# Optimization experiments

Hardware: AMD Instinct MI355X
Metric: run time of the kernel (lower is better)

## Reference

```python
import jax, jax.numpy as jnp
import numpy as np

B, HQ, HKV, D = 32, 32, 8, 128
BLOCK_SIZE, MAX_BLOCKS = 16, 128
NUM_BLOCKS = B * MAX_BLOCKS
LMAX = MAX_BLOCKS * BLOCK_SIZE  # 2048 max context per sequence
ROPE_BASE = 10000.0


def _rope(x, pos):
    """Apply rotary embedding. x: [B, H, D], pos: [B] int positions."""
    half = D // 2
    inv_freq = 1.0 / (ROPE_BASE ** (jnp.arange(0, D, 2, dtype=jnp.float32) / D))  # [D/2]
    freqs = pos.astype(jnp.float32)[:, None] * inv_freq[None, :]  # [B, D/2]
    emb = jnp.concatenate([freqs, freqs], axis=-1)                # [B, D]
    cos = jnp.cos(emb)[:, None, :]  # [B, 1, D]
    sin = jnp.sin(emb)[:, None, :]
    x1, x2 = x[..., :half], x[..., half:]
    rotated = jnp.concatenate([-x2, x1], axis=-1)
    return x * cos + rotated * sin


def setup_inputs() -> dict:
    key = jax.random.key(0)
    ks = jax.random.split(key, 6)
    query = jax.random.normal(ks[0], (B, HQ, D), jnp.float32)
    new_k = jax.random.normal(ks[1], (B, HKV, D), jnp.float32)
    new_v = jax.random.normal(ks[2], (B, HKV, D), jnp.float32)
    k_cache = jax.random.normal(ks[3], (NUM_BLOCKS, BLOCK_SIZE, HKV, D), jnp.float32)
    v_cache = jax.random.normal(ks[4], (NUM_BLOCKS, BLOCK_SIZE, HKV, D), jnp.float32)
    # each sequence owns a disjoint contiguous range of blocks
    block_table = jnp.arange(B * MAX_BLOCKS, dtype=jnp.int32).reshape(B, MAX_BLOCKS)
    context_lens = jax.random.randint(ks[5], (B,), 1, LMAX - 1).astype(jnp.int32)
    return dict(query=query, new_k=new_k, new_v=new_v, k_cache=k_cache,
                v_cache=v_cache, block_table=block_table, context_lens=context_lens)


def reference(query, new_k, new_v, k_cache, v_cache, block_table, context_lens):
    scale = 1.0 / D ** 0.5
    pos = context_lens  # new token position for each sequence, [B]

    # RoPE on the decode-step query and key (seq_len == 1 per sequence)
    q = _rope(query, pos)      # [B, HQ, D]
    k_new = _rope(new_k, pos)  # [B, HKV, D]

    # flatten paged cache to [NUM_BLOCKS*BLOCK_SIZE, HKV, D]
    kc = k_cache.reshape(-1, HKV, D)
    vc = v_cache.reshape(-1, HKV, D)

    # paged KV-cache append: slot = block_table[b, pos//bs]*bs + pos%bs
    blk_new = jnp.take_along_axis(block_table, (pos // BLOCK_SIZE)[:, None], axis=1)[:, 0]
    slot = blk_new * BLOCK_SIZE + pos % BLOCK_SIZE  # [B]
    kc = kc.at[slot].set(k_new)
    vc = vc.at[slot].set(new_v)

    # gather per-sequence K/V via block table: [B, LMAX, HKV, D]
    p = jnp.arange(LMAX, dtype=jnp.int32)
    blks = block_table[:, p // BLOCK_SIZE]                 # [B, LMAX]
    idx = blks * BLOCK_SIZE + (p % BLOCK_SIZE)[None, :]    # [B, LMAX]
    keys = kc[idx]
    vals = vc[idx]

    # GQA attention over valid context (lengths = context_lens + 1 after append)
    lens = pos + 1
    g = HQ // HKV
    qg = q.reshape(B, HKV, g, D)
    scores = jnp.einsum('bkgd,blkd->bkgl', qg, keys) * scale  # [B, HKV, g, LMAX]
    mask = p[None, :] < lens[:, None]  # [B, LMAX]
    scores = jnp.where(mask[:, None, None, :], scores, -jnp.inf)
    w = jax.nn.softmax(scores, axis=-1)
    out = jnp.einsum('bkgl,blkd->bkgd', w, vals)
    return out.reshape(B, HQ, D)
```

## Files before the change

### kernel.cpp

```cpp
#include <hip/hip_runtime.h>
#include <math.h>

#define BATCH 32
#define HQ 32
#define HKV 8
#define DHEAD 128
#define BS 16
#define MAXB 128
#define G 4
#define CHUNK 256
#define MAXCH 8
#define NW 4
#define NT (NW * 64)

#define NSLOT (BATCH * HKV * MAXCH)

typedef float v2f __attribute__((ext_vector_type(2)));

__device__ __forceinline__ v2f pk_fma(v2f a, v2f b, v2f c) {
    v2f d;
    asm("v_pk_fma_f32 %0, %1, %2, %3" : "=v"(d) : "v"(a), "v"(b), "v"(c));
    return d;
}
__device__ __forceinline__ v2f pk_mul(v2f a, v2f b) {
    v2f d;
    asm("v_pk_mul_f32 %0, %1, %2" : "=v"(d) : "v"(a), "v"(b));
    return d;
}

#define ROR4(N, x0, x1, x2, x3)                                                   \
    asm("s_nop 1\n\t"                                                             \
        "v_add_f32_dpp %0, %0, %0 row_ror:" #N " row_mask:0xf bank_mask:0xf\n\t"  \
        "v_add_f32_dpp %1, %1, %1 row_ror:" #N " row_mask:0xf bank_mask:0xf\n\t"  \
        "v_add_f32_dpp %2, %2, %2 row_ror:" #N " row_mask:0xf bank_mask:0xf\n\t"  \
        "v_add_f32_dpp %3, %3, %3 row_ror:" #N " row_mask:0xf bank_mask:0xf"      \
        : "+v"(x0), "+v"(x1), "+v"(x2), "+v"(x3))

__global__ __launch_bounds__(NT) void paged_attn_chunk(
    const float* __restrict__ query,
    const float* __restrict__ new_k,
    const float* __restrict__ new_v,
    const float* __restrict__ k_cache,
    const float* __restrict__ v_cache,
    const int*   __restrict__ block_table,
    const int*   __restrict__ context_lens,
    float*       __restrict__ wsacc,
    float*       __restrict__ wsl)
{
    const int c   = blockIdx.x & (MAXCH - 1);
    const int bkv = blockIdx.x >> 3;
    const int kv  = bkv & 7;
    const int b   = bkv >> 3;

    const int pos = context_lens[b];
    const int len = pos + 1;
    const int c0  = c * CHUNK;
    if (c0 >= len) return;

    const int tid  = threadIdx.x;
    const int w    = tid >> 6;
    const int lane = tid & 63;
    const int grp  = lane >> 4;
    const int sub  = lane & 15;

    __shared__ float s_cos[64], s_sin[64];
    __shared__ float s_q[G][DHEAD];
    __shared__ float s_knew[DHEAD], s_vnew[DHEAD];
    __shared__ int   s_bt[CHUNK / BS];
    __shared__ float s_wacc[NW][G][DHEAD];
    __shared__ float s_wl[NW][G];

    if (tid < 64) {
        float invf = exp2f((float)tid * -0.20762050593046014f);
        float ang  = (float)pos * invf;
        s_cos[tid] = cosf(ang);
        s_sin[tid] = sinf(ang);
    }
    __syncthreads();

    const float scale = 0.08838834764831845f;

    for (int idx = tid; idx < G * DHEAD; idx += NT) {
        int h = idx >> 7, d = idx & 127;
        const float* qp = query + ((size_t)b * HQ + kv * G + h) * DHEAD;
        float x = qp[d], r;
        if (d < 64) r = x * s_cos[d]      - qp[d + 64] * s_sin[d];
        else        r = x * s_cos[d - 64] + qp[d - 64] * s_sin[d - 64];
        s_q[h][d] = r * scale;
    }
    if (tid < DHEAD) {
        int d = tid;
        const float* kp = new_k + ((size_t)b * HKV + kv) * DHEAD;
        float x = kp[d], r;
        if (d < 64) r = x * s_cos[d]      - kp[d + 64] * s_sin[d];
        else        r = x * s_cos[d - 64] + kp[d - 64] * s_sin[d - 64];
        s_knew[d] = r;
    } else if (tid < 2 * DHEAD) {
        int d = tid - DHEAD;
        s_vnew[d] = new_v[((size_t)b * HKV + kv) * DHEAD + d];
    }
    if (tid < CHUNK / BS) s_bt[tid] = block_table[b * MAXB + (c0 >> 4) + tid];
    __syncthreads();

    v2f q2[G][4];
    #pragma unroll
    for (int h = 0; h < G; h++)
        #pragma unroll
        for (int j = 0; j < 4; j++)
            q2[h][j] = v2f{s_q[h][sub * 8 + 2 * j], s_q[h][sub * 8 + 2 * j + 1]};

    v2f acc2[G][4];
    float l[G];
    #pragma unroll
    for (int h = 0; h < G; h++) {
        l[h] = 0.f;
        #pragma unroll
        for (int j = 0; j < 4; j++) acc2[h][j] = v2f{0.f, 0.f};
    }

    const size_t lofs = (size_t)kv * DHEAD + sub * 8;

    const int base = c0 + w * 64;
    int rem = len - base;
    int a = rem < 0 ? 0 : (rem > 64 ? 64 : rem);
    int nfull = a >> 2;
    int tail  = a & 3;

#define BODY(GUARDED)                                                          \
    {                                                                          \
        int slot = w * 64 + it * 4 + grp;                                      \
        int pi   = c0 + slot;                                                  \
        bool act = !(GUARDED) || (grp < tail);                                 \
        v2f k2[4], u2[4];                                                      \
        _Pragma("unroll")                                                      \
        for (int j = 0; j < 4; j++) { k2[j] = v2f{0.f, 0.f}; u2[j] = v2f{0.f, 0.f}; } \
        if (act) {                                                             \
            int blk = s_bt[slot >> 4];                                         \
            size_t row = (size_t)blk * (BS * HKV * DHEAD)                      \
                       + (size_t)(slot & 15) * (HKV * DHEAD) + lofs;           \
            float4 ka = *(const float4*)(k_cache + row);                       \
            float4 kb = *(const float4*)(k_cache + row + 4);                   \
            float4 va = *(const float4*)(v_cache + row);                       \
            float4 vb = *(const float4*)(v_cache + row + 4);                   \
            if (pi == pos) {                                                   \
                ka = *(const float4*)(s_knew + sub * 8);                       \
                kb = *(const float4*)(s_knew + sub * 8 + 4);                   \
                va = *(const float4*)(s_vnew + sub * 8);                       \
                vb = *(const float4*)(s_vnew + sub * 8 + 4);                   \
            }                                                                  \
            k2[0] = v2f{ka.x, ka.y}; k2[1] = v2f{ka.z, ka.w};                  \
            k2[2] = v2f{kb.x, kb.y}; k2[3] = v2f{kb.z, kb.w};                  \
            u2[0] = v2f{va.x, va.y}; u2[1] = v2f{va.z, va.w};                  \
            u2[2] = v2f{vb.x, vb.y}; u2[3] = v2f{vb.z, vb.w};                  \
        }                                                                      \
        float dt0, dt1, dt2, dt3;                                              \
        {                                                                      \
            v2f d0 = pk_fma(q2[0][3], k2[3], pk_fma(q2[0][2], k2[2],           \
                     pk_fma(q2[0][1], k2[1], pk_mul(q2[0][0], k2[0]))));       \
            v2f d1 = pk_fma(q2[1][3], k2[3], pk_fma(q2[1][2], k2[2],           \
                     pk_fma(q2[1][1], k2[1], pk_mul(q2[1][0], k2[0]))));       \
            v2f d2 = pk_fma(q2[2][3], k2[3], pk_fma(q2[2][2], k2[2],           \
                     pk_fma(q2[2][1], k2[1], pk_mul(q2[2][0], k2[0]))));       \
            v2f d3 = pk_fma(q2[3][3], k2[3], pk_fma(q2[3][2], k2[2],           \
                     pk_fma(q2[3][1], k2[1], pk_mul(q2[3][0], k2[0]))));       \
            dt0 = d0.x + d0.y; dt1 = d1.x + d1.y;                              \
            dt2 = d2.x + d2.y; dt3 = d3.x + d3.y;                              \
        }                                                                      \
        ROR4(8, dt0, dt1, dt2, dt3);                                           \
        ROR4(4, dt0, dt1, dt2, dt3);                                           \
        ROR4(2, dt0, dt1, dt2, dt3);                                           \
        ROR4(1, dt0, dt1, dt2, dt3);                                           \
        if (act) {                                                             \
            float wg0 = __expf(dt0), wg1 = __expf(dt1);                        \
            float wg2 = __expf(dt2), wg3 = __expf(dt3);                        \
            l[0] += wg0; l[1] += wg1; l[2] += wg2; l[3] += wg3;                \
            v2f w0 = v2f{wg0, wg0}, w1 = v2f{wg1, wg1};                        \
            v2f w2 = v2f{wg2, wg2}, w3 = v2f{wg3, wg3};                        \
            _Pragma("unroll")                                                  \
            for (int j = 0; j < 4; j++) {                                      \
                acc2[0][j] = pk_fma(w0, u2[j], acc2[0][j]);                    \
                acc2[1][j] = pk_fma(w1, u2[j], acc2[1][j]);                    \
                acc2[2][j] = pk_fma(w2, u2[j], acc2[2][j]);                    \
                acc2[3][j] = pk_fma(w3, u2[j], acc2[3][j]);                    \
            }                                                                  \
        }                                                                      \
    }

    #pragma unroll 2
    for (int it = 0; it < nfull; it++) BODY(false)
    if (tail) { int it = nfull; BODY(true) }
#undef BODY

    #pragma unroll
    for (int h = 0; h < G; h++) {
        l[h] += __shfl_xor(l[h], 16, 64);
        l[h] += __shfl_xor(l[h], 32, 64);
        #pragma unroll
        for (int j = 0; j < 4; j++) {
            float ax = acc2[h][j].x, ay = acc2[h][j].y;
            ax += __shfl_xor(ax, 16, 64); ax += __shfl_xor(ax, 32, 64);
            ay += __shfl_xor(ay, 16, 64); ay += __shfl_xor(ay, 32, 64);
            acc2[h][j] = v2f{ax, ay};
        }
    }
    if (lane < 16) {
        #pragma unroll
        for (int h = 0; h < G; h++)
            #pragma unroll
            for (int j = 0; j < 4; j++) {
                s_wacc[w][h][sub * 8 + 2 * j]     = acc2[h][j].x;
                s_wacc[w][h][sub * 8 + 2 * j + 1] = acc2[h][j].y;
            }
    }
    if (lane == 0) {
        #pragma unroll
        for (int h = 0; h < G; h++) s_wl[w][h] = l[h];
    }
    __syncthreads();

    const size_t slot_base = (size_t)blockIdx.x * (G * DHEAD);
    for (int idx = tid; idx < G * DHEAD; idx += NT) {
        float s = s_wacc[0][idx >> 7][idx & 127] + s_wacc[1][idx >> 7][idx & 127]
                + s_wacc[2][idx >> 7][idx & 127] + s_wacc[3][idx >> 7][idx & 127];
        wsacc[slot_base + idx] = s;
    }
    if (tid < G) {
        wsl[(size_t)blockIdx.x * G + tid] =
            s_wl[0][tid] + s_wl[1][tid] + s_wl[2][tid] + s_wl[3][tid];
    }
}

__global__ __launch_bounds__(512) void paged_attn_combine(
    const int*   __restrict__ context_lens,
    const float* __restrict__ wsacc,
    const float* __restrict__ wsl,
    float*       __restrict__ out)
{
    const int bkv = blockIdx.x;
    const int kv  = bkv & 7;
    const int b   = bkv >> 3;
    const int t   = threadIdx.x;
    const int h   = t >> 7;
    const int d   = t & 127;

    const int len = context_lens[b] + 1;
    const int nch = (len + CHUNK - 1) >> 8;

    float asum = 0.f, lsum = 0.f;
    for (int cc = 0; cc < nch; cc++) {
        asum += wsacc[((size_t)bkv * MAXCH + cc) * (G * DHEAD) + t];
        lsum += wsl[((size_t)bkv * MAXCH + cc) * G + h];
    }
    out[((size_t)b * HQ + kv * G + h) * DHEAD + d] = asum / lsum;
}

extern "C" void kernel_launch(void* const* d_in, const int* in_sizes, int n_in,
                              void* d_out, int out_size, void* d_ws, size_t ws_size,
                              hipStream_t stream) {
    const float* query        = (const float*)d_in[0];
    const float* new_k        = (const float*)d_in[1];
    const float* new_v        = (const float*)d_in[2];
    const float* k_cache      = (const float*)d_in[3];
    const float* v_cache      = (const float*)d_in[4];
    const int*   block_table  = (const int*)d_in[5];
    const int*   context_lens = (const int*)d_in[6];
    float* out = (float*)d_out;

    float* wsacc = (float*)d_ws;
    float* wsl   = wsacc + (size_t)NSLOT * G * DHEAD;

    paged_attn_chunk<<<dim3(BATCH * HKV * MAXCH), dim3(NT), 0, stream>>>(
        query, new_k, new_v, k_cache, v_cache, block_table, context_lens,
        wsacc, wsl);
    paged_attn_combine<<<dim3(BATCH * HKV), dim3(512), 0, stream>>>(
        context_lens, wsacc, wsl, out);
}
```

Baseline: 72.49 us.

## Split RoPE prep into separate kernel, halve chunk size, software-pipeline KV loads

Moves the RoPE and scale setup for the query and new key/value into a separate prep kernel that writes to workspace, so the attention chunk kernel no longer recomputes sin/cos and skips the shared-memory staging and barriers. Chunk size drops from 256 to 128 with twice as many chunks, which gives more blocks and finer load balance. The chunk loop is fully unrolled with double-buffered K/V register loads, and the softmax uses raw exp2 with log2e folded into the scale. In exchange it adds a third kernel launch and more combine work per sequence, and masked lanes still issue loads past the context end.

```diff
diff --git a/kernel.cpp b/kernel.cpp
--- a/kernel.cpp
+++ b/kernel.cpp
@@ -8,12 +8,13 @@
 #define BS 16
 #define MAXB 128
 #define G 4
-#define CHUNK 256
-#define MAXCH 8
+#define CHUNK 128
+#define MAXCH 16
 #define NW 4
 #define NT (NW * 64)
 
 #define NSLOT (BATCH * HKV * MAXCH)
+#define NBKV  (BATCH * HKV)
 
 typedef float v2f __attribute__((ext_vector_type(2)));
 
@@ -26,6 +27,11 @@
     v2f d;
     asm("v_pk_mul_f32 %0, %1, %2" : "=v"(d) : "v"(a), "v"(b));
     return d;
+}
+__device__ __forceinline__ float fexp2(float x) {
+    float r;
+    asm("v_exp_f32 %0, %1" : "=v"(r) : "v"(x));
+    return r;
 }
 
 #define ROR4(N, x0, x1, x2, x3)                                                   \
@@ -36,26 +42,70 @@
         "v_add_f32_dpp %3, %3, %3 row_ror:" #N " row_mask:0xf bank_mask:0xf"      \
         : "+v"(x0), "+v"(x1), "+v"(x2), "+v"(x3))
 
-__global__ __launch_bounds__(NT) void paged_attn_chunk(
+__global__ __launch_bounds__(128) void paged_attn_prep(
     const float* __restrict__ query,
     const float* __restrict__ new_k,
     const float* __restrict__ new_v,
+    const int*   __restrict__ context_lens,
+    float* __restrict__ qs,
+    float* __restrict__ kn,
+    float* __restrict__ vn)
+{
+    const int bkv = blockIdx.x;
+    const int kv  = bkv & 7;
+    const int b   = bkv >> 3;
+    const int tid = threadIdx.x;
+
+    __shared__ float s_cos[64], s_sin[64];
+    const int pos = context_lens[b];
+    if (tid < 64) {
+        float invf = exp2f((float)tid * -0.20762050593046014f);
+        float ang  = (float)pos * invf;
+        s_cos[tid] = cosf(ang);
+        s_sin[tid] = sinf(ang);
+    }
+    __syncthreads();
+
+    const float scale = 0.08838834764831845f * 1.4426950408889634f;
+
+    for (int idx = tid; idx < G * DHEAD; idx += 128) {
+        int h = idx >> 7, d = idx & 127;
+        const float* qp = query + ((size_t)b * HQ + kv * G + h) * DHEAD;
+        float x = qp[d], r;
+        if (d < 64) r = x * s_cos[d]      - qp[d + 64] * s_sin[d];
+        else        r = x * s_cos[d - 64] + qp[d - 64] * s_sin[d - 64];
+        qs[(size_t)bkv * (G * DHEAD) + idx] = r * scale;
+    }
+    {
+        int d = tid;
+        const float* kp = new_k + ((size_t)b * HKV + kv) * DHEAD;
+        float x = kp[d], r;
+        if (d < 64) r = x * s_cos[d]      - kp[d + 64] * s_sin[d];
+        else        r = x * s_cos[d - 64] + kp[d - 64] * s_sin[d - 64];
+        kn[(size_t)bkv * DHEAD + d] = r;
+        vn[(size_t)bkv * DHEAD + d] = new_v[((size_t)b * HKV + kv) * DHEAD + d];
+    }
+}
+
+__global__ __launch_bounds__(NT) void paged_attn_chunk(
     const float* __restrict__ k_cache,
     const float* __restrict__ v_cache,
     const int*   __restrict__ block_table,
     const int*   __restrict__ context_lens,
+    const float* __restrict__ qs,
+    const float* __restrict__ kn,
+    const float* __restrict__ vn,
     float*       __restrict__ wsacc,
     float*       __restrict__ wsl)
 {
     const int c   = blockIdx.x & (MAXCH - 1);
-    const int bkv = blockIdx.x >> 3;
+    const int bkv = blockIdx.x >> 4;
     const int kv  = bkv & 7;
     const int b   = bkv >> 3;
 
     const int pos = context_lens[b];
-    const int len = pos + 1;
-    const int c0  = c * CHUNK;
-    if (c0 >= len) return;
+    const int c0  = c << 7;
+    if (c0 > pos) return;
 
     const int tid  = threadIdx.x;
     const int w    = tid >> 6;
@@ -63,51 +113,33 @@
     const int grp  = lane >> 4;
     const int sub  = lane & 15;
 
-    __shared__ float s_cos[64], s_sin[64];
-    __shared__ float s_q[G][DHEAD];
-    __shared__ float s_knew[DHEAD], s_vnew[DHEAD];
-    __shared__ int   s_bt[CHUNK / BS];
     __shared__ float s_wacc[NW][G][DHEAD];
     __shared__ float s_wl[NW][G];
 
-    if (tid < 64) {
-        float invf = exp2f((float)tid * -0.20762050593046014f);
-        float ang  = (float)pos * invf;
-        s_cos[tid] = cosf(ang);
-        s_sin[tid] = sinf(ang);
-    }
-    __syncthreads();
-
-    const float scale = 0.08838834764831845f;
-
-    for (int idx = tid; idx < G * DHEAD; idx += NT) {
-        int h = idx >> 7, d = idx & 127;
-        const float* qp = query + ((size_t)b * HQ + kv * G + h) * DHEAD;
-        float x = qp[d], r;
-        if (d < 64) r = x * s_cos[d]      - qp[d + 64] * s_sin[d];
-        else        r = x * s_cos[d - 64] + qp[d - 64] * s_sin[d - 64];
-        s_q[h][d] = r * scale;
-    }
-    if (tid < DHEAD) {
-        int d = tid;
-        const float* kp = new_k + ((size_t)b * HKV + kv) * DHEAD;
-        float x = kp[d], r;
-        if (d < 64) r = x * s_cos[d]      - kp[d + 64] * s_sin[d];
-        else        r = x * s_cos[d - 64] + kp[d - 64] * s_sin[d - 64];
-        s_knew[d] = r;
-    } else if (tid < 2 * DHEAD) {
-        int d = tid - DHEAD;
-        s_vnew[d] = new_v[((size_t)b * HKV + kv) * DHEAD + d];
-    }
-    if (tid < CHUNK / BS) s_bt[tid] = block_table[b * MAXB + (c0 >> 4) + tid];
-    __syncthreads();
-
     v2f q2[G][4];
+    const float* qb = qs + (size_t)bkv * (G * DHEAD) + sub * 8;
     #pragma unroll
-    for (int h = 0; h < G; h++)
-        #pragma unroll
-        for (int j = 0; j < 4; j++)
-            q2[h][j] = v2f{s_q[h][sub * 8 + 2 * j], s_q[h][sub * 8 + 2 * j + 1]};
+    for (int h = 0; h < G; h++) {
+        float4 qa = *(const float4*)(qb + h * DHEAD);
+        float4 qc = *(const float4*)(qb + h * DHEAD + 4);
+        q2[h][0] = v2f{qa.x, qa.y}; q2[h][1] = v2f{qa.z, qa.w};
+        q2[h][2] = v2f{qc.x, qc.y}; q2[h][3] = v2f{qc.z, qc.w};
+    }
+
+    const int tb  = b * MAXB + (c0 >> 4) + w * 2;
+    const int bt0 = __builtin_amdgcn_readfirstlane(block_table[tb]);
+    const int bt1 = __builtin_amdgcn_readfirstlane(block_table[tb + 1]);
+
+    const int poff = grp * (HKV * DHEAD) + kv * DHEAD + sub * 8;
+    const float* kb0 = k_cache + (size_t)bt0 * (BS * HKV * DHEAD) + poff;
+    const float* kb1 = k_cache + (size_t)bt1 * (BS * HKV * DHEAD) + poff;
+    const float* vb0 = v_cache + (size_t)bt0 * (BS * HKV * DHEAD) + poff;
+    const float* vb1 = v_cache + (size_t)bt1 * (BS * HKV * DHEAD) + poff;
+
+    const float* knp = kn + (size_t)bkv * DHEAD + sub * 8;
+    const float* vnp = vn + (size_t)bkv * DHEAD + sub * 8;
+
+    const int p0 = c0 + w * 32 + grp;
 
     v2f acc2[G][4];
     float l[G];
@@ -118,78 +150,79 @@
         for (int j = 0; j < 4; j++) acc2[h][j] = v2f{0.f, 0.f};
     }
 
-    const size_t lofs = (size_t)kv * DHEAD + sub * 8;
-
-    const int base = c0 + w * 64;
-    int rem = len - base;
-    int a = rem < 0 ? 0 : (rem > 64 ? 64 : rem);
-    int nfull = a >> 2;
-    int tail  = a & 3;
-
-#define BODY(GUARDED)                                                          \
-    {                                                                          \
-        int slot = w * 64 + it * 4 + grp;                                      \
-        int pi   = c0 + slot;                                                  \
-        bool act = !(GUARDED) || (grp < tail);                                 \
-        v2f k2[4], u2[4];                                                      \
-        _Pragma("unroll")                                                      \
-        for (int j = 0; j < 4; j++) { k2[j] = v2f{0.f, 0.f}; u2[j] = v2f{0.f, 0.f}; } \
-        if (act) {                                                             \
-            int blk = s_bt[slot >> 4];                                         \
-            size_t row = (size_t)blk * (BS * HKV * DHEAD)                      \
-                       + (size_t)(slot & 15) * (HKV * DHEAD) + lofs;           \
-            float4 ka = *(const float4*)(k_cache + row);                       \
-            float4 kb = *(const float4*)(k_cache + row + 4);                   \
-            float4 va = *(const float4*)(v_cache + row);                       \
-            float4 vb = *(const float4*)(v_cache + row + 4);                   \
-            if (pi == pos) {                                                   \
-                ka = *(const float4*)(s_knew + sub * 8);                       \
-                kb = *(const float4*)(s_knew + sub * 8 + 4);                   \
-                va = *(const float4*)(s_vnew + sub * 8);                       \
-                vb = *(const float4*)(s_vnew + sub * 8 + 4);                   \
-            }                                                                  \
-            k2[0] = v2f{ka.x, ka.y}; k2[1] = v2f{ka.z, ka.w};                  \
-            k2[2] = v2f{kb.x, kb.y}; k2[3] = v2f{kb.z, kb.w};                  \
-            u2[0] = v2f{va.x, va.y}; u2[1] = v2f{va.z, va.w};                  \
-            u2[2] = v2f{vb.x, vb.y}; u2[3] = v2f{vb.z, vb.w};                  \
+    float4 kaA, kbA, vaA, vbA;
+    float4 kaB, kbB, vaB, vbB;
+
+#define LOADSET(KA, KB, VA, VB, IT) do {                                       \
+        const float* kp_ = ((IT) < 4 ? kb0 : kb1) + ((IT) & 3) * 4096;         \
+        const float* vp_ = ((IT) < 4 ? vb0 : vb1) + ((IT) & 3) * 4096;         \
+        KA = *(const float4*)kp_;  KB = *(const float4*)(kp_ + 4);             \
+        VA = *(const float4*)vp_;  VB = *(const float4*)(vp_ + 4);             \
+    } while (0)
+
+#define COMPSET(KA, KB, VA, VB, IT) do {                                       \
+        const int pi_ = p0 + (IT) * 4;                                         \
+        if (__builtin_expect(pi_ == pos, 0)) {      \
+            KA = *(const float4*)(knp);  KB = *(const float4*)(knp + 4);       \
+            VA = *(const float4*)(vnp);  VB = *(const float4*)(vnp + 4);       \
         }                                                                      \
-        float dt0, dt1, dt2, dt3;                                              \
-        {                                                                      \
-            v2f d0 = pk_fma(q2[0][3], k2[3], pk_fma(q2[0][2], k2[2],           \
-                     pk_fma(q2[0][1], k2[1], pk_mul(q2[0][0], k2[0]))));       \
-            v2f d1 = pk_fma(q2[1][3], k2[3], pk_fma(q2[1][2], k2[2],           \
-                     pk_fma(q2[1][1], k2[1], pk_mul(q2[1][0], k2[0]))));       \
-            v2f d2 = pk_fma(q2[2][3], k2[3], pk_fma(q2[2][2], k2[2],           \
-                     pk_fma(q2[2][1], k2[1], pk_mul(q2[2][0], k2[0]))));       \
-            v2f d3 = pk_fma(q2[3][3], k2[3], pk_fma(q2[3][2], k2[2],           \
-                     pk_fma(q2[3][1], k2[1], pk_mul(q2[3][0], k2[0]))));       \
-            dt0 = d0.x + d0.y; dt1 = d1.x + d1.y;                              \
-            dt2 = d2.x + d2.y; dt3 = d3.x + d3.y;                              \
-        }                                                                      \
+        v2f k0_ = v2f{KA.x, KA.y}, k1_ = v2f{KA.z, KA.w};                      \
+        v2f k2_ = v2f{KB.x, KB.y}, k3_ = v2f{KB.z, KB.w};                      \
+        v2f d0_ = pk_fma(q2[0][3], k3_, pk_fma(q2[0][2], k2_,                  \
+                  pk_fma(q2[0][1], k1_, pk_mul(q2[0][0], k0_))));              \
+        v2f d1_ = pk_fma(q2[1][3], k3_, pk_fma(q2[1][2], k2_,                  \
+                  pk_fma(q2[1][1], k1_, pk_mul(q2[1][0], k0_))));              \
+        v2f d2_ = pk_fma(q2[2][3], k3_, pk_fma(q2[2][2], k2_,                  \
+                  pk_fma(q2[2][1], k1_, pk_mul(q2[2][0], k0_))));              \
+        v2f d3_ = pk_fma(q2[3][3], k3_, pk_fma(q2[3][2], k2_,                  \
+                  pk_fma(q2[3][1], k1_, pk_mul(q2[3][0], k0_))));              \
+        float dt0 = d0_.x + d0_.y, dt1 = d1_.x + d1_.y;                        \
+        float dt2 = d2_.x + d2_.y, dt3 = d3_.x + d3_.y;                        \
         ROR4(8, dt0, dt1, dt2, dt3);                                           \
         ROR4(4, dt0, dt1, dt2, dt3);                                           \
         ROR4(2, dt0, dt1, dt2, dt3);                                           \
         ROR4(1, dt0, dt1, dt2, dt3);                                           \
-        if (act) {                                                             \
-            float wg0 = __expf(dt0), wg1 = __expf(dt1);                        \
-            float wg2 = __expf(dt2), wg3 = __expf(dt3);                        \
-            l[0] += wg0; l[1] += wg1; l[2] += wg2; l[3] += wg3;                \
-            v2f w0 = v2f{wg0, wg0}, w1 = v2f{wg1, wg1};                        \
-            v2f w2 = v2f{wg2, wg2}, w3 = v2f{wg3, wg3};                        \
-            _Pragma("unroll")                                                  \
-            for (int j = 0; j < 4; j++) {                                      \
-                acc2[0][j] = pk_fma(w0, u2[j], acc2[0][j]);                    \
-                acc2[1][j] = pk_fma(w1, u2[j], acc2[1][j]);                    \
-                acc2[2][j] = pk_fma(w2, u2[j], acc2[2][j]);                    \
-                acc2[3][j] = pk_fma(w3, u2[j], acc2[3][j]);                    \
-            }                                                                  \
-        }                                                                      \
-    }
-
-    #pragma unroll 2
-    for (int it = 0; it < nfull; it++) BODY(false)
-    if (tail) { int it = nfull; BODY(true) }
-#undef BODY
+        const bool act_ = pi_ <= pos;                                          \
+        float wg0 = act_ ? fexp2(dt0) : 0.f;                                   \
+        float wg1 = act_ ? fexp2(dt1) : 0.f;                                   \
+        float wg2 = act_ ? fexp2(dt2) : 0.f;                                   \
+        float wg3 = act_ ? fexp2(dt3) : 0.f;                                   \
+        l[0] += wg0; l[1] += wg1; l[2] += wg2; l[3] += wg3;                    \
+        v2f u0_ = v2f{VA.x, VA.y}, u1_ = v2f{VA.z, VA.w};                      \
+        v2f u2_ = v2f{VB.x, VB.y}, u3_ = v2f{VB.z, VB.w};                      \
+        v2f w0_ = v2f{wg0, wg0}, w1_ = v2f{wg1, wg1};                          \
+        v2f w2_ = v2f{wg2, wg2}, w3_ = v2f{wg3, wg3};                          \
+        acc2[0][0] = pk_fma(w0_, u0_, acc2[0][0]);                             \
+        acc2[0][1] = pk_fma(w0_, u1_, acc2[0][1]);                             \
+        acc2[0][2] = pk_fma(w0_, u2_, acc2[0][2]);                             \
+        acc2[0][3] = pk_fma(w0_, u3_, acc2[0][3]);                             \
+        acc2[1][0] = pk_fma(w1_, u0_, acc2[1][0]);                             \
+        acc2[1][1] = pk_fma(w1_, u1_, acc2[1][1]);                             \
+        acc2[1][2] = pk_fma(w1_, u2_, acc2[1][2]);                             \
+        acc2[1][3] = pk_fma(w1_, u3_, acc2[1][3]);                             \
+        acc2[2][0] = pk_fma(w2_, u0_, acc2[2][0]);                             \
+        acc2[2][1] = pk_fma(w2_, u1_, acc2[2][1]);                             \
+        acc2[2][2] = pk_fma(w2_, u2_, acc2[2][2]);                             \
+        acc2[2][3] = pk_fma(w2_, u3_, acc2[2][3]);                             \
+        acc2[3][0] = pk_fma(w3_, u0_, acc2[3][0]);                             \
+        acc2[3][1] = pk_fma(w3_, u1_, acc2[3][1]);                             \
+        acc2[3][2] = pk_fma(w3_, u2_, acc2[3][2]);                             \
+        acc2[3][3] = pk_fma(w3_, u3_, acc2[3][3]);                             \
+    } while (0)
+
+    LOADSET(kaA, kbA, vaA, vbA, 0);
+    LOADSET(kaB, kbB, vaB, vbB, 1);
+    COMPSET(kaA, kbA, vaA, vbA, 0);  LOADSET(kaA, kbA, vaA, vbA, 2);
+    COMPSET(kaB, kbB, vaB, vbB, 1);  LOADSET(kaB, kbB, vaB, vbB, 3);
+    COMPSET(kaA, kbA, vaA, vbA, 2);  LOADSET(kaA, kbA, vaA, vbA, 4);
+    COMPSET(kaB, kbB, vaB, vbB, 3);  LOADSET(kaB, kbB, vaB, vbB, 5);
+    COMPSET(kaA, kbA, vaA, vbA, 4);  LOADSET(kaA, kbA, vaA, vbA, 6);
+    COMPSET(kaB, kbB, vaB, vbB, 5);  LOADSET(kaB, kbB, vaB, vbB, 7);
+    COMPSET(kaA, kbA, vaA, vbA, 6);
+    COMPSET(kaB, kbB, vaB, vbB, 7);
+
+#undef LOADSET
+#undef COMPSET
 
     #pragma unroll
     for (int h = 0; h < G; h++) {
@@ -244,7 +277,7 @@
     const int d   = t & 127;
 
     const int len = context_lens[b] + 1;
-    const int nch = (len + CHUNK - 1) >> 8;
+    const int nch = (len + CHUNK - 1) >> 7;
 
     float asum = 0.f, lsum = 0.f;
     for (int cc = 0; cc < nch; cc++) {
@@ -268,10 +301,14 @@
 
     float* wsacc = (float*)d_ws;
     float* wsl   = wsacc + (size_t)NSLOT * G * DHEAD;
-
-    paged_attn_chunk<<<dim3(BATCH * HKV * MAXCH), dim3(NT), 0, stream>>>(
-        query, new_k, new_v, k_cache, v_cache, block_table, context_lens,
-        wsacc, wsl);
-    paged_attn_combine<<<dim3(BATCH * HKV), dim3(512), 0, stream>>>(
+    float* qs    = wsl + (size_t)NSLOT * G;
+    float* kn    = qs + (size_t)NBKV * G * DHEAD;
+    float* vn    = kn + (size_t)NBKV * DHEAD;
+
+    paged_attn_prep<<<dim3(NBKV), dim3(128), 0, stream>>>(
+        query, new_k, new_v, context_lens, qs, kn, vn);
+    paged_attn_chunk<<<dim3(NSLOT), dim3(NT), 0, stream>>>(
+        k_cache, v_cache, block_table, context_lens, qs, kn, vn, wsacc, wsl);
+    paged_attn_combine<<<dim3(NBKV), dim3(512), 0, stream>>>(
         context_lens, wsacc, wsl, out);
 }
```

Result: slower. 85.29 us (+17.7%).
